# Optimization experiments

Hardware: AMD Instinct MI355X
Metric: run time of the kernel (lower is better)

Reference implementation:

```python
import jax, jax.numpy as jnp
import numpy as np

N_NODES = 100000
N_EDGES = 1600000
D_FEAT = 256


def _glorot(key, shape):
    fan_in = shape[0]
    return jax.random.normal(key, shape, jnp.float32) * (1.0 / np.sqrt(fan_in))


def setup_inputs() -> dict:
    key = jax.random.key(0)
    ks = jax.random.split(key, 8)
    return {
        "x": jax.random.normal(ks[0], (N_NODES, D_FEAT), jnp.float32),
        "edge_index": jax.random.randint(ks[1], (2, N_EDGES), 0, N_NODES, jnp.int32),
        "w1": _glorot(ks[2], (D_FEAT, 64)),
        "b1": jnp.zeros((64,), jnp.float32),
        "w2": _glorot(ks[3], (64, 32)),
        "b2": jnp.zeros((32,), jnp.float32),
        "wf1": _glorot(ks[4], (32, 16)),
        "bf1": jnp.zeros((16,), jnp.float32),
        "wf2": _glorot(ks[5], (16, 1)),
        "bf2": jnp.zeros((1,), jnp.float32),
    }


def reference(x, edge_index, w1, b1, w2, b2, wf1, bf1, wf2, bf2):
    n = x.shape[0]
    # GCNConv: add self-loops, symmetric D^{-1/2}(A+I)D^{-1/2} normalization
    loops = jnp.arange(n, dtype=edge_index.dtype)
    src = jnp.concatenate([edge_index[0], loops])  # message sources
    dst = jnp.concatenate([edge_index[1], loops])  # aggregation targets
    deg = jax.ops.segment_sum(jnp.ones_like(dst, x.dtype), dst, num_segments=n)
    dinv = jnp.where(deg > 0, jax.lax.rsqrt(jnp.maximum(deg, 1.0)), 0.0)
    norm = dinv[src] * dinv[dst]  # [E+N]

    def gcn_conv(h, W, b):
        hw = h @ W                                   # dense transform first (smaller msg dim)
        msg = hw[src] * norm[:, None]                # gather + scale
        return jax.ops.segment_sum(msg, dst, num_segments=n) + b  # scatter-add

    h = jax.nn.relu(gcn_conv(x, w1, b1))
    h = jax.nn.relu(gcn_conv(h, w2, b2))
    h = jax.nn.relu(h @ wf1 + bf1)
    out = h @ wf2 + bf2
    return out.squeeze(-1)  # [N]
```

## Files before the change

kernel.cpp:

```cpp
#include <hip/hip_runtime.h>
#include <cstdint>
#include <cstddef>

#define N_NODES 100000
#define N_EDGES 1600000

#define BKB   7
#define BN    128
#define NBK   782
#define NPB   256
#define EPB   ((N_EDGES + NPB - 1) / NPB)
#define NSLOT (NBK * NPB)
#define NSB   ((NSLOT + 1023) / 1024)
#define ES_CAP (N_EDGES + NBK * 1024 + 64)
#define EB_CAP 2560

typedef __attribute__((ext_vector_type(8))) short bf16x8;
typedef __attribute__((ext_vector_type(4))) float f32x4;

__device__ __forceinline__ float b2f(unsigned short u) {
    return __uint_as_float(((unsigned)u) << 16);
}
__device__ __forceinline__ unsigned short f2b(float f) {
    unsigned x = __float_as_uint(f);
    return (unsigned short)((x + 0x7FFFu + ((x >> 16) & 1u)) >> 16);
}

__device__ __forceinline__ void split8a(const float* f, bf16x8& hi, bf16x8& lo) {
#pragma unroll
    for (int j = 0; j < 8; ++j) {
        unsigned u = __float_as_uint(f[j]);
        hi[j] = (short)(u >> 16);
        float l = f[j] - __uint_as_float(u & 0xFFFF0000u);
        lo[j] = (short)(__float_as_uint(l) >> 16);
    }
}
__device__ __forceinline__ void split8(const float4& a0, const float4& a1,
                                       bf16x8& hi, bf16x8& lo) {
    float f[8] = {a0.x, a0.y, a0.z, a0.w, a1.x, a1.y, a1.z, a1.w};
    split8a(f, hi, lo);
}

__device__ __forceinline__ void bsum_excl(const int* __restrict__ bsum, int* pe) {
    int t = threadIdx.x;
    int v = (t < NSB) ? bsum[t] : 0;
    pe[t] = v;
    __syncthreads();
    for (int o = 1; o < 256; o <<= 1) {
        int a = (t >= o) ? pe[t - o] : 0;
        __syncthreads();
        pe[t] += a;
        __syncthreads();
    }
    pe[t] -= v;
    __syncthreads();
}


__global__ __launch_bounds__(256) void k_hist(const int* __restrict__ dst,
                                              int* __restrict__ gcnt,
                                              unsigned short* __restrict__ hwb1,
                                              unsigned short* __restrict__ hwb2, int E) {
    __shared__ int lh[NBK];
    int t = threadIdx.x, bid = blockIdx.x;
    if (bid == 0) {
        if (t < 64) hwb1[(size_t)N_NODES * 64 + t] = 0;
        else if (t < 96) hwb2[(size_t)N_NODES * 32 + (t - 64)] = 0;
    }
    for (int i = t; i < NBK; i += 256) lh[i] = 0;
    __syncthreads();
    int e0 = bid * EPB, e1 = min(E, e0 + EPB);
    for (int e = e0 + t; e < e1; e += 256) atomicAdd(&lh[dst[e] >> BKB], 1);
    __syncthreads();
    for (int b = t; b < NBK; b += 256) gcnt[b * NPB + bid] = lh[b];
}

__global__ __launch_bounds__(1024) void k_scanA(int* __restrict__ g,
                                                int* __restrict__ bsum, int ntot) {
    __shared__ int s[1024];
    int t = threadIdx.x;
    int i = blockIdx.x * 1024 + t;
    int v = (i < ntot) ? g[i] : 0;
    s[t] = v;
    __syncthreads();
    for (int o = 1; o < 1024; o <<= 1) {
        int a = (t >= o) ? s[t - o] : 0;
        __syncthreads();
        s[t] += a;
        __syncthreads();
    }
    if (i < ntot) g[i] = s[t] - v;
    if (t == 1023) bsum[blockIdx.x] = s[1023];
}

__global__ __launch_bounds__(256) void k_partition(const int* __restrict__ src,
                                                   const int* __restrict__ dst,
                                                   const int* __restrict__ g,
                                                   const int* __restrict__ bsum,
                                                   unsigned* __restrict__ ebuf, int E) {
    __shared__ int lcur[NBK];
    __shared__ int pe[256];
    int t = threadIdx.x, bid = blockIdx.x;
    bsum_excl(bsum, pe);
    for (int b = t; b < NBK; b += 256) {
        int slot = b * NPB + bid;
        lcur[b] = g[slot] + pe[slot >> 10];
    }
    __syncthreads();
    int e0 = bid * EPB, e1 = min(E, e0 + EPB);
    for (int e = e0 + t; e < e1; e += 256) {
        int d = dst[e];
        int b = d >> BKB;
        int p = atomicAdd(&lcur[b], 1);
        ebuf[p] = (unsigned)src[e] | ((unsigned)(d & (BN - 1)) << 20);
    }
}

__global__ __launch_bounds__(256) void k_bucket_csr(const int* __restrict__ g,
                                                    const int* __restrict__ bsum,
                                                    const unsigned* __restrict__ ebuf,
                                                    int* __restrict__ cnt,
                                                    float* __restrict__ dinv,
                                                    int* __restrict__ off,
                                                    int* __restrict__ es, int n) {
    __shared__ unsigned eb[EB_CAP];
    __shared__ int lc[BN];
    __shared__ int ss[BN];
    __shared__ int lo[BN];
    __shared__ int lcur[BN];
    __shared__ int pe[256];
    int b = blockIdx.x, t = threadIdx.x;
    bsum_excl(bsum, pe);
    int s0 = b * NPB;
    int rstart = g[s0] + pe[s0 >> 10];
    int rend;
    if (b == NBK - 1) rend = N_EDGES;
    else { int s1 = (b + 1) * NPB; rend = g[s1] + pe[s1 >> 10]; }
    int m = rend - rstart;
    int ms = min(m, EB_CAP);
    int wstart = ((rstart + 7) & ~7) + b * 1024;
    if (t < BN) lc[t] = 0;
    for (int i = t; i < ms; i += 256) eb[i] = ebuf[rstart + i];
    __syncthreads();
    for (int e = t; e < m; e += 256) {
        unsigned u = (e < ms) ? eb[e] : ebuf[rstart + e];
        atomicAdd(&lc[(int)(u >> 20)], 1);
    }
    __syncthreads();
    int v = 0, vp = 0;
    if (t < BN) {
        v = lc[t];
        vp = (v + 7) & ~7;
        ss[t] = vp;
    }
    __syncthreads();
    for (int o = 1; o < BN; o <<= 1) {
        int a = (t >= o && t < BN) ? ss[t - o] : 0;
        __syncthreads();
        if (t < BN) ss[t] += a;
        __syncthreads();
    }
    if (t < BN) {
        lo[t] = ss[t] - vp;
        lcur[t] = 0;
        int node = b * BN + t;
        if (node < n) {
            cnt[node] = vp;
            dinv[node] = rsqrtf((float)v + 1.0f);
            off[node] = wstart + lo[t];
        }
    }
    __syncthreads();
    for (int e = t; e < m; e += 256) {
        unsigned u = (e < ms) ? eb[e] : ebuf[rstart + e];
        int l = (int)(u >> 20);
        int p = atomicAdd(&lcur[l], 1);
        es[wstart + lo[l] + p] = (int)(u & 0xFFFFFu);
    }
    if (t < BN)
        for (int q = v; q < vp; ++q) es[wstart + lo[t] + q] = N_NODES;
}


__global__ __launch_bounds__(256) void k_gemm1_mfma(const float* __restrict__ x,
                                                    const float* __restrict__ w,
                                                    const float* __restrict__ dinv,
                                                    unsigned short* __restrict__ out, int M) {
    __shared__ unsigned short Bhi[32 * 64 * 8];
    __shared__ unsigned short Blo[32 * 64 * 8];
    int t = threadIdx.x;
    int wave = t >> 6, lane = t & 63;

    {
        int c = t & 63;
        int kg0 = t >> 6;
#pragma unroll
        for (int i = 0; i < 8; ++i) {
            int kgrp = kg0 + i * 4;
            bf16x8 h8, l8;
#pragma unroll
            for (int j = 0; j < 8; ++j) {
                float f = w[(size_t)(kgrp * 8 + j) * 64 + c];
                unsigned u = __float_as_uint(f);
                h8[j] = (short)(u >> 16);
                float l = f - __uint_as_float(u & 0xFFFF0000u);
                l8[j] = (short)(__float_as_uint(l) >> 16);
            }
            *(bf16x8*)&Bhi[(kgrp * 64 + c) * 8] = h8;
            *(bf16x8*)&Blo[(kgrp * 64 + c) * 8] = l8;
        }
    }
    __syncthreads();

    int row0w = blockIdx.x * 64 + wave * 16;
    int r = row0w + (lane & 15); if (r >= M) r = M - 1;
    const float* xr = x + (size_t)r * 256 + (lane >> 4) * 8;

    f32x4 acc[4] = {{0.f,0.f,0.f,0.f},{0.f,0.f,0.f,0.f},{0.f,0.f,0.f,0.f},{0.f,0.f,0.f,0.f}};

#pragma unroll
    for (int kf = 0; kf < 8; ++kf) {
        float4 a0 = *(const float4*)(xr + kf * 32);
        float4 a1 = *(const float4*)(xr + kf * 32 + 4);
        bf16x8 ahi, alo;
        split8(a0, a1, ahi, alo);
        int kgrpR = kf * 4 + (lane >> 4);
#pragma unroll
        for (int cf = 0; cf < 4; ++cf) {
            bf16x8 bhi = *(const bf16x8*)&Bhi[(kgrpR * 64 + cf * 16 + (lane & 15)) * 8];
            bf16x8 blo = *(const bf16x8*)&Blo[(kgrpR * 64 + cf * 16 + (lane & 15)) * 8];
            acc[cf] = __builtin_amdgcn_mfma_f32_16x16x32_bf16(ahi, bhi, acc[cf], 0, 0, 0);
            acc[cf] = __builtin_amdgcn_mfma_f32_16x16x32_bf16(ahi, blo, acc[cf], 0, 0, 0);
            acc[cf] = __builtin_amdgcn_mfma_f32_16x16x32_bf16(alo, bhi, acc[cf], 0, 0, 0);
        }
    }

#pragma unroll
    for (int j = 0; j < 4; ++j) {
        int rr = row0w + (lane >> 4) * 4 + j;
        if (rr < M) {
            float s = dinv[rr];
#pragma unroll
            for (int cf = 0; cf < 4; ++cf)
                out[(size_t)rr * 64 + cf * 16 + (lane & 15)] = f2b(acc[cf][j] * s);
        }
    }
}


__global__ __launch_bounds__(256) void k_agg1_gemm2(const unsigned short* __restrict__ hwb,
                                                    const float* __restrict__ dinv,
                                                    const int* __restrict__ cnt,
                                                    const int* __restrict__ off,
                                                    const int* __restrict__ es,
                                                    const float* __restrict__ bias,
                                                    const float* __restrict__ w2,
                                                    unsigned short* __restrict__ out) {
    __shared__ float hs[16][68];
    int t = threadIdx.x;
    int wv = t >> 6, lane = t & 63;
    int node0 = blockIdx.x * 16;
    float bl = bias[lane];

    float dn[4], a0[4], a1[4];
    const int* ep[4];
    int mp[4];
#pragma unroll
    for (int i = 0; i < 4; ++i) {
        int node = node0 + wv * 4 + i;
        dn[i] = dinv[node];
        a0[i] = b2f(hwb[(size_t)node * 64 + lane]);
        a1[i] = 0.0f;
        ep[i] = es + off[node];
        mp[i] = cnt[node];
    }
    int mmax = max(max(mp[0], mp[1]), max(mp[2], mp[3]));
    for (int j = 0; j < mmax; j += 8) {
#pragma unroll
        for (int i = 0; i < 4; ++i) {
            if (j < mp[i]) {
                int4 e0 = *(const int4*)&ep[i][j];
                int4 e1 = *(const int4*)&ep[i][j + 4];
                float v0 = b2f(hwb[(size_t)e0.x * 64 + lane]);
                float v1 = b2f(hwb[(size_t)e0.y * 64 + lane]);
                float v2 = b2f(hwb[(size_t)e0.z * 64 + lane]);
                float v3 = b2f(hwb[(size_t)e0.w * 64 + lane]);
                float v4 = b2f(hwb[(size_t)e1.x * 64 + lane]);
                float v5 = b2f(hwb[(size_t)e1.y * 64 + lane]);
                float v6 = b2f(hwb[(size_t)e1.z * 64 + lane]);
                float v7 = b2f(hwb[(size_t)e1.w * 64 + lane]);
                a0[i] += (v0 + v1) + (v2 + v3);
                a1[i] += (v4 + v5) + (v6 + v7);
            }
        }
    }
#pragma unroll
    for (int i = 0; i < 4; ++i)
        hs[wv * 4 + i][lane] = fmaxf(fmaf(dn[i], a0[i] + a1[i], bl), 0.0f);
    __syncthreads();

    if (wv < 2) {
        int colbase = wv * 16;
        int r = lane & 15;
        int kg = lane >> 4;
        f32x4 acc = {0.f, 0.f, 0.f, 0.f};
#pragma unroll
        for (int ks = 0; ks < 2; ++ks) {
            float a[8], b[8];
#pragma unroll
            for (int j = 0; j < 8; ++j) {
                int k = ks * 32 + kg * 8 + j;
                a[j] = hs[r][k];
                b[j] = w2[(size_t)k * 32 + colbase + r];
            }
            bf16x8 ahi, alo, bhi, blo;
            split8a(a, ahi, alo);
            split8a(b, bhi, blo);
            acc = __builtin_amdgcn_mfma_f32_16x16x32_bf16(ahi, bhi, acc, 0, 0, 0);
            acc = __builtin_amdgcn_mfma_f32_16x16x32_bf16(ahi, blo, acc, 0, 0, 0);
            acc = __builtin_amdgcn_mfma_f32_16x16x32_bf16(alo, bhi, acc, 0, 0, 0);
        }
#pragma unroll
        for (int reg = 0; reg < 4; ++reg) {
            int row = kg * 4 + reg;
            int nd = node0 + row;
            out[(size_t)nd * 32 + colbase + r] = f2b(acc[reg] * dinv[nd]);
        }
    }
}


__global__ __launch_bounds__(256) void k_agg2_mlp(const unsigned short* __restrict__ hwb,
                                                  const float* __restrict__ dinv,
                                                  const int* __restrict__ cnt,
                                                  const int* __restrict__ off,
                                                  const int* __restrict__ es,
                                                  const float* __restrict__ bias2,
                                                  const float* __restrict__ wf1,
                                                  const float* __restrict__ bf1,
                                                  const float* __restrict__ wf2,
                                                  const float* __restrict__ bf2,
                                                  float* __restrict__ out) {
    __shared__ float hs[8][33];
    __shared__ float W1[512];
    __shared__ float B1[16];
    __shared__ float W2[16];
    int t = threadIdx.x;
    W1[t] = wf1[t];
    W1[t + 256] = wf1[t + 256];
    if (t < 16) { B1[t] = bf1[t]; W2[t] = wf2[t]; }

    int node0 = blockIdx.x * 8;
    int nl = t >> 5;
    int c = t & 31;
    int node = node0 + nl;
    float dn = dinv[node];
    float acc0 = b2f(hwb[(size_t)node * 32 + c]);
    float acc1 = 0.0f;
    const int* ep = es + off[node];
    int mp = cnt[node];
    for (int j = 0; j < mp; j += 8) {
        int4 e0 = *(const int4*)&ep[j];
        int4 e1 = *(const int4*)&ep[j + 4];
        float v0 = b2f(hwb[(size_t)e0.x * 32 + c]);
        float v1 = b2f(hwb[(size_t)e0.y * 32 + c]);
        float v2 = b2f(hwb[(size_t)e0.z * 32 + c]);
        float v3 = b2f(hwb[(size_t)e0.w * 32 + c]);
        float v4 = b2f(hwb[(size_t)e1.x * 32 + c]);
        float v5 = b2f(hwb[(size_t)e1.y * 32 + c]);
        float v6 = b2f(hwb[(size_t)e1.z * 32 + c]);
        float v7 = b2f(hwb[(size_t)e1.w * 32 + c]);
        acc0 += (v0 + v1) + (v2 + v3);
        acc1 += (v4 + v5) + (v6 + v7);
    }
    hs[nl][c] = fmaxf(fmaf(dn, acc0 + acc1, bias2[c]), 0.0f);
    __syncthreads();
    if (t < 128) {
        int nn = t >> 4, jj = t & 15;
        float s = B1[jj];
#pragma unroll
        for (int k = 0; k < 32; ++k) s += hs[nn][k] * W1[k * 16 + jj];
        float p = fmaxf(s, 0.0f) * W2[jj];
        p += __shfl_xor(p, 1);
        p += __shfl_xor(p, 2);
        p += __shfl_xor(p, 4);
        p += __shfl_xor(p, 8);
        if (jj == 0) out[node0 + nn] = p + bf2[0];
    }
}


extern "C" void kernel_launch(void* const* d_in, const int* in_sizes, int n_in,
                              void* d_out, int out_size, void* d_ws, size_t ws_size,
                              hipStream_t stream) {
    const float* x   = (const float*)d_in[0];
    const int*   ei  = (const int*)d_in[1];
    const float* w1  = (const float*)d_in[2];
    const float* b1  = (const float*)d_in[3];
    const float* w2  = (const float*)d_in[4];
    const float* b2  = (const float*)d_in[5];
    const float* wf1 = (const float*)d_in[6];
    const float* bf1 = (const float*)d_in[7];
    const float* wf2 = (const float*)d_in[8];
    const float* bf2 = (const float*)d_in[9];

    const int n = N_NODES;
    const int E = N_EDGES;
    const int* srcp = ei;
    const int* dstp = ei + E;

    char* p = (char*)d_ws;
    auto take = [&](size_t bytes) {
        char* r = p;
        p += (bytes + 255) & ~(size_t)255;
        return r;
    };
    float* dinv = (float*)take((size_t)n * 4);
    int*   cnt  = (int*)take((size_t)n * 4);
    int*   off  = (int*)take((size_t)n * 4);
    int*   gcnt = (int*)take((size_t)NSLOT * 4);
    int*   bsum = (int*)take(1024);
    int*   es   = (int*)take((size_t)ES_CAP * 4);
    unsigned short* hwb1 = (unsigned short*)take((size_t)(n + 1) * 64 * 2);
    unsigned short* hwb2 = (unsigned short*)take((size_t)(n + 1) * 32 * 2);
    unsigned* ebuf = (unsigned*)hwb1;

    k_hist<<<NPB, 256, 0, stream>>>(dstp, gcnt, hwb1, hwb2, E);
    k_scanA<<<NSB, 1024, 0, stream>>>(gcnt, bsum, NSLOT);
    k_partition<<<NPB, 256, 0, stream>>>(srcp, dstp, gcnt, bsum, ebuf, E);
    k_bucket_csr<<<NBK, 256, 0, stream>>>(gcnt, bsum, ebuf, cnt, dinv, off, es, n);

    k_gemm1_mfma<<<(n + 63) / 64, 256, 0, stream>>>(x, w1, dinv, hwb1, n);
    k_agg1_gemm2<<<n / 16, 256, 0, stream>>>(hwb1, dinv, cnt, off, es, b1, w2, hwb2);
    k_agg2_mlp<<<n / 8, 256, 0, stream>>>(hwb2, dinv, cnt, off, es, b2,
                                          wf1, bf1, wf2, bf2, (float*)d_out);
}
```

Baseline: 161.6 us.

## Fuse histogram with GEMM1 and move source-degree scaling into aggregation

The first GEMM no longer depends on dinv, so it is merged into the histogram kernel as extra blocks. This removes a launch and lets the dense transform overlap with the edge-bucketing pass. To make that possible, the per-source dinv scale is applied inside the layer-1 aggregation through an extra gathered dinv load per edge, with a padding entry for the dummy node. The edge buffer gets its own workspace allocation instead of aliasing hwb1, and x is read with nontemporal loads. The cost is more scattered loads in agg1, more workspace memory, and a larger mixed-role kernel.

```diff
diff --git a/kernel.cpp b/kernel.cpp
--- a/kernel.cpp
+++ b/kernel.cpp
@@ -14,6 +14,7 @@
 #define NSB   ((NSLOT + 1023) / 1024)
 #define ES_CAP (N_EDGES + NBK * 1024 + 64)
 #define EB_CAP 2560
+#define GEMM1_BLOCKS ((N_NODES + 63) / 64)
 
 typedef __attribute__((ext_vector_type(8))) short bf16x8;
 typedef __attribute__((ext_vector_type(4))) float f32x4;
@@ -35,9 +36,8 @@
         lo[j] = (short)(__float_as_uint(l) >> 16);
     }
 }
-__device__ __forceinline__ void split8(const float4& a0, const float4& a1,
-                                       bf16x8& hi, bf16x8& lo) {
-    float f[8] = {a0.x, a0.y, a0.z, a0.w, a1.x, a1.y, a1.z, a1.w};
+__device__ __forceinline__ void split8v(f32x4 a0, f32x4 a1, bf16x8& hi, bf16x8& lo) {
+    float f[8] = {a0[0], a0[1], a0[2], a0[3], a1[0], a1[1], a1[2], a1[3]};
     split8a(f, hi, lo);
 }
 
@@ -57,22 +57,88 @@
 }
 
 
-__global__ __launch_bounds__(256) void k_hist(const int* __restrict__ dst,
-                                              int* __restrict__ gcnt,
-                                              unsigned short* __restrict__ hwb1,
-                                              unsigned short* __restrict__ hwb2, int E) {
-    __shared__ int lh[NBK];
+__global__ __launch_bounds__(256) void k_hist_gemm1(const int* __restrict__ dst,
+                                                    int* __restrict__ gcnt,
+                                                    const float* __restrict__ x,
+                                                    const float* __restrict__ w,
+                                                    unsigned short* __restrict__ hwb1,
+                                                    unsigned short* __restrict__ hwb2,
+                                                    float* __restrict__ dinv, int M) {
+    __shared__ unsigned short Bhi[32 * 64 * 8];
+    __shared__ unsigned short Blo[32 * 64 * 8];
     int t = threadIdx.x, bid = blockIdx.x;
-    if (bid == 0) {
-        if (t < 64) hwb1[(size_t)N_NODES * 64 + t] = 0;
-        else if (t < 96) hwb2[(size_t)N_NODES * 32 + (t - 64)] = 0;
-    }
-    for (int i = t; i < NBK; i += 256) lh[i] = 0;
-    __syncthreads();
-    int e0 = bid * EPB, e1 = min(E, e0 + EPB);
-    for (int e = e0 + t; e < e1; e += 256) atomicAdd(&lh[dst[e] >> BKB], 1);
-    __syncthreads();
-    for (int b = t; b < NBK; b += 256) gcnt[b * NPB + bid] = lh[b];
+
+    if (bid < NPB) {
+        int* lh = (int*)Bhi;
+        if (bid == 0) {
+            if (t < 64) hwb1[(size_t)N_NODES * 64 + t] = 0;
+            else if (t < 96) hwb2[(size_t)N_NODES * 32 + (t - 64)] = 0;
+            else if (t == 96) dinv[N_NODES] = 0.0f;
+        }
+        for (int i = t; i < NBK; i += 256) lh[i] = 0;
+        __syncthreads();
+        int e0 = bid * EPB, e1 = min(N_EDGES, e0 + EPB);
+        for (int e = e0 + t; e < e1; e += 256) atomicAdd(&lh[dst[e] >> BKB], 1);
+        __syncthreads();
+        for (int b = t; b < NBK; b += 256) gcnt[b * NPB + bid] = lh[b];
+        return;
+    }
+
+    int tile = bid - NPB;
+    int wave = t >> 6, lane = t & 63;
+    {
+        int c = t & 63;
+        int kg0 = t >> 6;
+#pragma unroll
+        for (int i = 0; i < 8; ++i) {
+            int kgrp = kg0 + i * 4;
+            bf16x8 h8, l8;
+#pragma unroll
+            for (int j = 0; j < 8; ++j) {
+                float f = w[(size_t)(kgrp * 8 + j) * 64 + c];
+                unsigned u = __float_as_uint(f);
+                h8[j] = (short)(u >> 16);
+                float l = f - __uint_as_float(u & 0xFFFF0000u);
+                l8[j] = (short)(__float_as_uint(l) >> 16);
+            }
+            *(bf16x8*)&Bhi[(kgrp * 64 + c) * 8] = h8;
+            *(bf16x8*)&Blo[(kgrp * 64 + c) * 8] = l8;
+        }
+    }
+    __syncthreads();
+
+    int row0w = tile * 64 + wave * 16;
+    int r = row0w + (lane & 15); if (r >= M) r = M - 1;
+    const float* xr = x + (size_t)r * 256 + (lane >> 4) * 8;
+
+    f32x4 acc[4] = {{0.f,0.f,0.f,0.f},{0.f,0.f,0.f,0.f},{0.f,0.f,0.f,0.f},{0.f,0.f,0.f,0.f}};
+
+#pragma unroll
+    for (int kf = 0; kf < 8; ++kf) {
+        f32x4 a0 = __builtin_nontemporal_load((const f32x4*)(xr + kf * 32));
+        f32x4 a1 = __builtin_nontemporal_load((const f32x4*)(xr + kf * 32 + 4));
+        bf16x8 ahi, alo;
+        split8v(a0, a1, ahi, alo);
+        int kgrpR = kf * 4 + (lane >> 4);
+#pragma unroll
+        for (int cf = 0; cf < 4; ++cf) {
+            bf16x8 bhi = *(const bf16x8*)&Bhi[(kgrpR * 64 + cf * 16 + (lane & 15)) * 8];
+            bf16x8 blo = *(const bf16x8*)&Blo[(kgrpR * 64 + cf * 16 + (lane & 15)) * 8];
+            acc[cf] = __builtin_amdgcn_mfma_f32_16x16x32_bf16(ahi, bhi, acc[cf], 0, 0, 0);
+            acc[cf] = __builtin_amdgcn_mfma_f32_16x16x32_bf16(ahi, blo, acc[cf], 0, 0, 0);
+            acc[cf] = __builtin_amdgcn_mfma_f32_16x16x32_bf16(alo, bhi, acc[cf], 0, 0, 0);
+        }
+    }
+
+#pragma unroll
+    for (int j = 0; j < 4; ++j) {
+        int rr = row0w + (lane >> 4) * 4 + j;
+        if (rr < M) {
+#pragma unroll
+            for (int cf = 0; cf < 4; ++cf)
+                hwb1[(size_t)rr * 64 + cf * 16 + (lane & 15)] = f2b(acc[cf][j]);
+        }
+    }
 }
 
 __global__ __launch_bounds__(1024) void k_scanA(int* __restrict__ g,
@@ -182,72 +248,6 @@
 }
 
 
-__global__ __launch_bounds__(256) void k_gemm1_mfma(const float* __restrict__ x,
-                                                    const float* __restrict__ w,
-                                                    const float* __restrict__ dinv,
-                                                    unsigned short* __restrict__ out, int M) {
-    __shared__ unsigned short Bhi[32 * 64 * 8];
-    __shared__ unsigned short Blo[32 * 64 * 8];
-    int t = threadIdx.x;
-    int wave = t >> 6, lane = t & 63;
-
-    {
-        int c = t & 63;
-        int kg0 = t >> 6;
-#pragma unroll
-        for (int i = 0; i < 8; ++i) {
-            int kgrp = kg0 + i * 4;
-            bf16x8 h8, l8;
-#pragma unroll
-            for (int j = 0; j < 8; ++j) {
-                float f = w[(size_t)(kgrp * 8 + j) * 64 + c];
-                unsigned u = __float_as_uint(f);
-                h8[j] = (short)(u >> 16);
-                float l = f - __uint_as_float(u & 0xFFFF0000u);
-                l8[j] = (short)(__float_as_uint(l) >> 16);
-            }
-            *(bf16x8*)&Bhi[(kgrp * 64 + c) * 8] = h8;
-            *(bf16x8*)&Blo[(kgrp * 64 + c) * 8] = l8;
-        }
-    }
-    __syncthreads();
-
-    int row0w = blockIdx.x * 64 + wave * 16;
-    int r = row0w + (lane & 15); if (r >= M) r = M - 1;
-    const float* xr = x + (size_t)r * 256 + (lane >> 4) * 8;
-
-    f32x4 acc[4] = {{0.f,0.f,0.f,0.f},{0.f,0.f,0.f,0.f},{0.f,0.f,0.f,0.f},{0.f,0.f,0.f,0.f}};
-
-#pragma unroll
-    for (int kf = 0; kf < 8; ++kf) {
-        float4 a0 = *(const float4*)(xr + kf * 32);
-        float4 a1 = *(const float4*)(xr + kf * 32 + 4);
-        bf16x8 ahi, alo;
-        split8(a0, a1, ahi, alo);
-        int kgrpR = kf * 4 + (lane >> 4);
-#pragma unroll
-        for (int cf = 0; cf < 4; ++cf) {
-            bf16x8 bhi = *(const bf16x8*)&Bhi[(kgrpR * 64 + cf * 16 + (lane & 15)) * 8];
-            bf16x8 blo = *(const bf16x8*)&Blo[(kgrpR * 64 + cf * 16 + (lane & 15)) * 8];
-            acc[cf] = __builtin_amdgcn_mfma_f32_16x16x32_bf16(ahi, bhi, acc[cf], 0, 0, 0);
-            acc[cf] = __builtin_amdgcn_mfma_f32_16x16x32_bf16(ahi, blo, acc[cf], 0, 0, 0);
-            acc[cf] = __builtin_amdgcn_mfma_f32_16x16x32_bf16(alo, bhi, acc[cf], 0, 0, 0);
-        }
-    }
-
-#pragma unroll
-    for (int j = 0; j < 4; ++j) {
-        int rr = row0w + (lane >> 4) * 4 + j;
-        if (rr < M) {
-            float s = dinv[rr];
-#pragma unroll
-            for (int cf = 0; cf < 4; ++cf)
-                out[(size_t)rr * 64 + cf * 16 + (lane & 15)] = f2b(acc[cf][j] * s);
-        }
-    }
-}
-
-
 __global__ __launch_bounds__(256) void k_agg1_gemm2(const unsigned short* __restrict__ hwb,
                                                     const float* __restrict__ dinv,
                                                     const int* __restrict__ cnt,
@@ -269,7 +269,7 @@
     for (int i = 0; i < 4; ++i) {
         int node = node0 + wv * 4 + i;
         dn[i] = dinv[node];
-        a0[i] = b2f(hwb[(size_t)node * 64 + lane]);
+        a0[i] = dn[i] * b2f(hwb[(size_t)node * 64 + lane]);
         a1[i] = 0.0f;
         ep[i] = es + off[node];
         mp[i] = cnt[node];
@@ -281,6 +281,8 @@
             if (j < mp[i]) {
                 int4 e0 = *(const int4*)&ep[i][j];
                 int4 e1 = *(const int4*)&ep[i][j + 4];
+                float w0 = dinv[e0.x], w1 = dinv[e0.y], w2v = dinv[e0.z], w3 = dinv[e0.w];
+                float w4 = dinv[e1.x], w5 = dinv[e1.y], w6 = dinv[e1.z], w7 = dinv[e1.w];
                 float v0 = b2f(hwb[(size_t)e0.x * 64 + lane]);
                 float v1 = b2f(hwb[(size_t)e0.y * 64 + lane]);
                 float v2 = b2f(hwb[(size_t)e0.z * 64 + lane]);
@@ -289,8 +291,8 @@
                 float v5 = b2f(hwb[(size_t)e1.y * 64 + lane]);
                 float v6 = b2f(hwb[(size_t)e1.z * 64 + lane]);
                 float v7 = b2f(hwb[(size_t)e1.w * 64 + lane]);
-                a0[i] += (v0 + v1) + (v2 + v3);
-                a1[i] += (v4 + v5) + (v6 + v7);
+                a0[i] += (w0 * v0 + w1 * v1) + (w2v * v2 + w3 * v3);
+                a1[i] += (w4 * v4 + w5 * v5) + (w6 * v6 + w7 * v7);
             }
         }
     }
@@ -415,22 +417,22 @@
         p += (bytes + 255) & ~(size_t)255;
         return r;
     };
-    float* dinv = (float*)take((size_t)n * 4);
+    float* dinv = (float*)take((size_t)(n + 1) * 4);
     int*   cnt  = (int*)take((size_t)n * 4);
     int*   off  = (int*)take((size_t)n * 4);
     int*   gcnt = (int*)take((size_t)NSLOT * 4);
     int*   bsum = (int*)take(1024);
     int*   es   = (int*)take((size_t)ES_CAP * 4);
+    unsigned* ebuf = (unsigned*)take((size_t)E * 4);
     unsigned short* hwb1 = (unsigned short*)take((size_t)(n + 1) * 64 * 2);
     unsigned short* hwb2 = (unsigned short*)take((size_t)(n + 1) * 32 * 2);
-    unsigned* ebuf = (unsigned*)hwb1;
-
-    k_hist<<<NPB, 256, 0, stream>>>(dstp, gcnt, hwb1, hwb2, E);
+
+    k_hist_gemm1<<<NPB + GEMM1_BLOCKS, 256, 0, stream>>>(dstp, gcnt, x, w1,
+                                                         hwb1, hwb2, dinv, n);
     k_scanA<<<NSB, 1024, 0, stream>>>(gcnt, bsum, NSLOT);
     k_partition<<<NPB, 256, 0, stream>>>(srcp, dstp, gcnt, bsum, ebuf, E);
     k_bucket_csr<<<NBK, 256, 0, stream>>>(gcnt, bsum, ebuf, cnt, dinv, off, es, n);
 
-    k_gemm1_mfma<<<(n + 63) / 64, 256, 0, stream>>>(x, w1, dinv, hwb1, n);
     k_agg1_gemm2<<<n / 16, 256, 0, stream>>>(hwb1, dinv, cnt, off, es, b1, w2, hwb2);
     k_agg2_mlp<<<n / 8, 256, 0, stream>>>(hwb2, dinv, cnt, off, es, b2,
                                           wf1, bf1, wf2, bf2, (float*)d_out);
```

New measurement: 182.8 us. +13.1%, slower.
